# Performance work log

Hardware: AMD Instinct MI355X
Metric: run time of the kernel (lower is better)

## Reference

```python
import jax, jax.numpy as jnp
import numpy as np

LOD = 64          # latent observation dim
LSD = 2 * LOD     # latent state dim
BW = 3            # bandwidth
NB = 15           # num basis
B = 4096          # batch
H = 64            # hidden units of coefficient net

# band-structure indices (static, computed once)
_mask = np.triu(np.ones((LOD, LOD), np.float32), -BW) * np.tril(np.ones((LOD, LOD), np.float32), BW)
IDX0, IDX1 = np.where(_mask == 1)
DIAG_IDX = np.where(IDX0 == IDX1)[0]
NE = IDX0.shape[0]  # = 436 for lod=64, bw=3


def setup_inputs() -> dict:
    key = jax.random.key(0)
    ks = jax.random.split(key, 20)
    inp = {
        'prior_mean': jax.random.normal(ks[0], (B, LSD), jnp.float32),
        'cov_u': jax.random.uniform(ks[1], (B, LOD), jnp.float32) + 0.1,
        'cov_l': jax.random.uniform(ks[2], (B, LOD), jnp.float32) + 0.1,
        'cov_s': 0.1 * jax.random.uniform(ks[3], (B, LOD), jnp.float32),
        'obs': jax.random.normal(ks[4], (B, LOD), jnp.float32),
        'obs_var': jax.random.uniform(ks[5], (B, LOD), jnp.float32) + 0.1,
        # coefficient net params (Linear(LSD,H)-Tanh-Linear(H,H)-Tanh-Linear(H,NB)-Softmax)
        'W1': 0.05 * jax.random.normal(ks[6], (H, LSD), jnp.float32),
        'b1': jnp.zeros((H,), jnp.float32),
        'W2': 0.05 * jax.random.normal(ks[7], (H, H), jnp.float32),
        'b2': jnp.zeros((H,), jnp.float32),
        'W3': 0.05 * jax.random.normal(ks[8], (NB, H), jnp.float32),
        'b3': jnp.zeros((NB,), jnp.float32),
    }
    # transition basis matrices, flat band entries [NB, NE]
    tm11 = 0.02 * jax.random.normal(ks[9], (NB, NE), jnp.float32)
    tm12 = 0.02 * jax.random.normal(ks[10], (NB, NE), jnp.float32)
    tm12 = tm12.at[:, DIAG_IDX].add(0.2)
    tm21 = 0.02 * jax.random.normal(ks[11], (NB, NE), jnp.float32)
    tm21 = tm21.at[:, DIAG_IDX].add(-0.2)
    tm22 = 0.02 * jax.random.normal(ks[12], (NB, NE), jnp.float32)
    inp['tm11_basis'] = tm11
    inp['tm12_basis'] = tm12
    inp['tm21_basis'] = tm21
    inp['tm22_basis'] = tm22
    # log transition noise, init at var_activation_inverse(0.1) = log(exp(0.1)-1)
    inp['log_trans_noise'] = jnp.full((1, LSD), np.log(np.exp(0.1) - 1.0), jnp.float32)
    return inp


def _bmv(mat, vec):
    return jnp.einsum('bij,bj->bi', mat, vec)


def _unflatten_tm(flat):
    # flat: [B, NE] -> banded [B, LOD, LOD]
    tm = jnp.zeros((flat.shape[0], LOD, LOD), flat.dtype)
    return tm.at[:, IDX0, IDX1].set(flat)


def reference(prior_mean, cov_u, cov_l, cov_s, obs, obs_var,
              W1, b1, W2, b2, W3, b3,
              tm11_basis, tm12_basis, tm21_basis, tm22_basis, log_trans_noise):
    # ---- update (Kalman-style, factorized diagonal covariance) ----
    denom = cov_u + obs_var
    q_upper = cov_u / denom
    q_lower = cov_s / denom
    residual = obs - prior_mean[:, :LOD]
    post_mean = prior_mean + jnp.concatenate([q_upper * residual, q_lower * residual], -1)
    covar_factor = 1.0 - q_upper
    post_cu = covar_factor * cov_u
    post_cl = cov_l - q_lower * cov_s
    post_cs = covar_factor * cov_s

    # ---- coefficient net: MLP + softmax -> basis mixing coefficients ----
    h = jnp.tanh(post_mean @ W1.T + b1)
    h = jnp.tanh(h @ W2.T + b2)
    coeff = jax.nn.softmax(h @ W3.T + b3, axis=-1)  # [B, NB]

    # ---- locally-linear transition model ----
    tm11_flat = jnp.einsum('bk,ke->be', coeff, tm11_basis).at[:, DIAG_IDX].add(1.0)
    tm12_flat = jnp.einsum('bk,ke->be', coeff, tm12_basis)
    tm21_flat = jnp.einsum('bk,ke->be', coeff, tm21_basis)
    tm22_flat = jnp.einsum('bk,ke->be', coeff, tm22_basis).at[:, DIAG_IDX].add(1.0)
    tm11 = _unflatten_tm(tm11_flat)
    tm12 = _unflatten_tm(tm12_flat)
    tm21 = _unflatten_tm(tm21_flat)
    tm22 = _unflatten_tm(tm22_flat)

    trans_cov = jnp.log(jnp.exp(log_trans_noise) + 1.0)  # var_activation (softplus)
    tcu = trans_cov[:, :LOD]
    tcl = trans_cov[:, LOD:]

    # ---- predict ----
    mu = post_mean[:, :LOD]
    ml = post_mean[:, LOD:]
    next_mean = jnp.concatenate([_bmv(tm11, mu) + _bmv(tm12, ml),
                                 _bmv(tm21, mu) + _bmv(tm22, ml)], -1)
    # dadat(A, d) = bmv(A^2, d); dadbt(A, d, B) = bmv(A*B, d)
    next_cu = (_bmv(jnp.square(tm11), post_cu) + 2.0 * _bmv(tm11 * tm12, post_cs)
               + _bmv(jnp.square(tm12), post_cl) + tcu)
    next_cl = (_bmv(jnp.square(tm21), post_cu) + 2.0 * _bmv(tm21 * tm22, post_cs)
               + _bmv(jnp.square(tm22), post_cl) + tcl)
    next_cs = (_bmv(tm21 * tm11, post_cu) + _bmv(tm22 * tm11, post_cs)
               + _bmv(tm21 * tm12, post_cs) + _bmv(tm22 * tm12, post_cl))

    return (post_mean, post_cu, post_cl, post_cs, next_mean, next_cu, next_cl, next_cs)
```

## Files before the change

kernel.cpp:

```cpp
#include <hip/hip_runtime.h>
#include <math.h>

#define O_PM   0
#define O_PCU  524288
#define O_PCL  786432
#define O_PCS  1048576
#define O_NM   1310720
#define O_NCU  1835008
#define O_NCL  2097152
#define O_NCS  2359296

#define TM_S   1748
#define L_W1   0
#define L_W2   4864
#define L_W3   7680
#define L_TM   0
#define L_BAST 13984
#define L_PMB  27968
#define L_H1   29184
#define L_H2   29888
#define L_COEF 30592
#define L_PMF  30752
#define L_CUF  32800
#define L_CLF  33824
#define L_CSF  34848
#define L_TOT  35872

typedef short s8v __attribute__((ext_vector_type(8)));
typedef short s4v __attribute__((ext_vector_type(4)));
typedef float f4v __attribute__((ext_vector_type(4)));

__device__ __forceinline__ unsigned pk2(float a, float b) {
    unsigned ua = __float_as_uint(a), ub = __float_as_uint(b);
    ua += 0x7fffu + ((ua >> 16) & 1u);
    ub += 0x7fffu + ((ub >> 16) & 1u);
    return (ua >> 16) | (ub & 0xffff0000u);
}
__device__ __forceinline__ unsigned short tobf(float a) {
    unsigned ua = __float_as_uint(a);
    ua += 0x7fffu + ((ua >> 16) & 1u);
    return (unsigned short)(ua >> 16);
}
__device__ __forceinline__ float frombf(unsigned short u) {
    return __uint_as_float(((unsigned)u) << 16);
}
__device__ __forceinline__ float lo16(unsigned w) { return __uint_as_float(w << 16); }
__device__ __forceinline__ float hi16(unsigned w) { return __uint_as_float(w & 0xffff0000u); }
__device__ __forceinline__ float frcp(float x) { return __builtin_amdgcn_rcpf(x); }
__device__ __forceinline__ float ftanh(float x) {
    float e = __expf(2.f * x);
    return 1.f - 2.f * frcp(e + 1.f);
}
#define SWZ(v, imm) __uint_as_float((unsigned)__builtin_amdgcn_ds_swizzle((int)__float_as_uint(v), imm))

#if __has_builtin(__builtin_amdgcn_mfma_f32_16x16x16_bf16)
#define MFMA16(A,B,C) __builtin_amdgcn_mfma_f32_16x16x16_bf16(A,B,C,0,0,0)
#define HAVE_MFMA16 1
#elif __has_builtin(__builtin_amdgcn_mfma_f32_16x16x16bf16_1k)
#define MFMA16(A,B,C) __builtin_amdgcn_mfma_f32_16x16x16bf16_1k(A,B,C,0,0,0)
#define HAVE_MFMA16 1
#else
#define MFMA16(A,B,C) (C)
#define HAVE_MFMA16 1
#endif

__global__ __launch_bounds__(1024, 4)
void rkn_kernel(const float* __restrict__ prior_mean,
                const float* __restrict__ cov_u,
                const float* __restrict__ cov_l,
                const float* __restrict__ cov_s,
                const float* __restrict__ obs,
                const float* __restrict__ obs_var,
                const float* __restrict__ W1,
                const float* __restrict__ b1,
                const float* __restrict__ W2,
                const float* __restrict__ b2,
                const float* __restrict__ W3,
                const float* __restrict__ b3,
                const float* __restrict__ tm11b,
                const float* __restrict__ tm12b,
                const float* __restrict__ tm21b,
                const float* __restrict__ tm22b,
                const float* __restrict__ ltn,
                float* __restrict__ out)
{
    __shared__ __align__(16) unsigned smem[L_TOT];

    const int tid  = threadIdx.x;
    const int wid  = tid >> 6;
    const int lane = tid & 63;
    const int lrow = lane & 15;
    const int lkg  = lane >> 4;

    {
#pragma unroll
        for (int it = 0; it < 2; ++it) {
            const int idx = it * 1024 + tid;
            const float4 v = ((const float4*)W1)[idx];
            const int j = idx >> 5, kq = idx & 31;
            unsigned* d = smem + (L_W1 + j * 76 + kq * 2);
            d[0] = pk2(v.x, v.y); d[1] = pk2(v.z, v.w);
        }
        {
            const int idx = tid;
            const float4 v = ((const float4*)W2)[idx];
            const int j = idx >> 4, kq = idx & 15;
            unsigned* d = smem + (L_W2 + j * 44 + kq * 2);
            d[0] = pk2(v.x, v.y); d[1] = pk2(v.z, v.w);
        }
        if (tid < 240) {
            const float4 v = ((const float4*)W3)[tid];
            const int j = tid >> 4, kq = tid & 15;
            unsigned* d = smem + (L_W3 + j * 44 + kq * 2);
            d[0] = pk2(v.x, v.y); d[1] = pk2(v.z, v.w);
        } else if (tid < 284) {
            smem[L_W3 + 15 * 44 + (tid - 240)] = 0u;
        }
    }

    if (tid < 512) {
        const int prow  = tid >> 5;
        const int pd    = (tid & 31) << 1;
        const int grow1 = blockIdx.x * 16 + prow;
        const float2 cu2 = *(const float2*)(cov_u   + grow1 * 64 + pd);
        const float2 cl2 = *(const float2*)(cov_l   + grow1 * 64 + pd);
        const float2 cs2 = *(const float2*)(cov_s   + grow1 * 64 + pd);
        const float2 ob2 = *(const float2*)(obs     + grow1 * 64 + pd);
        const float2 ov2 = *(const float2*)(obs_var + grow1 * 64 + pd);
        const float2 pu2 = *(const float2*)(prior_mean + grow1 * 128 + pd);
        const float2 pl2 = *(const float2*)(prior_mean + grow1 * 128 + 64 + pd);

        const float i0 = frcp(cu2.x + ov2.x), i1 = frcp(cu2.y + ov2.y);
        const float qu0 = cu2.x * i0, qu1 = cu2.y * i1;
        const float ql0 = cs2.x * i0, ql1 = cs2.y * i1;
        const float r0 = ob2.x - pu2.x, r1 = ob2.y - pu2.y;
        const float pmu0 = pu2.x + qu0 * r0, pmu1 = pu2.y + qu1 * r1;
        const float pml0 = pl2.x + ql0 * r0, pml1 = pl2.y + ql1 * r1;
        const float cf0 = 1.f - qu0, cf1 = 1.f - qu1;
        const float pcu0 = cf0 * cu2.x, pcu1 = cf1 * cu2.y;
        const float pcl0 = cl2.x - ql0 * cs2.x, pcl1 = cl2.y - ql1 * cs2.y;
        const float pcs0 = cf0 * cs2.x, pcs1 = cf1 * cs2.y;

        *(float2*)(out + O_PM  + grow1 * 128 + pd)      = make_float2(pmu0, pmu1);
        *(float2*)(out + O_PM  + grow1 * 128 + 64 + pd) = make_float2(pml0, pml1);
        *(float2*)(out + O_PCU + grow1 * 64 + pd) = make_float2(pcu0, pcu1);
        *(float2*)(out + O_PCL + grow1 * 64 + pd) = make_float2(pcl0, pcl1);
        *(float2*)(out + O_PCS + grow1 * 64 + pd) = make_float2(pcs0, pcs1);

        smem[L_PMB + prow * 76 + (pd >> 1)]      = pk2(pmu0, pmu1);
        smem[L_PMB + prow * 76 + 32 + (pd >> 1)] = pk2(pml0, pml1);
        *(float2*)((float*)(smem + L_PMF) + prow * 128 + pd)      = make_float2(pmu0, pmu1);
        *(float2*)((float*)(smem + L_PMF) + prow * 128 + 64 + pd) = make_float2(pml0, pml1);
        *(float2*)((float*)(smem + L_CUF) + prow * 64 + pd) = make_float2(pcu0, pcu1);
        *(float2*)((float*)(smem + L_CLF) + prow * 64 + pd) = make_float2(pcl0, pcl1);
        *(float2*)((float*)(smem + L_CSF) + prow * 64 + pd) = make_float2(pcs0, pcs1);
    }

    const float tcu = __logf(__expf(ltn[lane]) + 1.f);
    const float tcl = __logf(__expf(ltn[64 + lane]) + 1.f);

    __syncthreads();

    const int t2 = tid - 256;
    const int ms = t2 & 3;
    const float* bps = (ms == 0) ? tm11b : (ms == 1) ? tm12b : (ms == 2) ? tm21b : tm22b;

    if (wid < 4) {
        const int w = wid;
        f4v acc = {0.f, 0.f, 0.f, 0.f};
#pragma unroll
        for (int s = 0; s < 4; ++s) {
            s8v a = *(const s8v*)(smem + L_PMB + lrow * 76 + s * 16 + lkg * 4);
            s8v b = *(const s8v*)(smem + L_W1 + (w * 16 + lrow) * 76 + s * 16 + lkg * 4);
            acc = __builtin_amdgcn_mfma_f32_16x16x32_bf16(a, b, acc, 0, 0, 0);
        }
        const float bc1 = b1[w * 16 + lrow];
        unsigned short* h1u = (unsigned short*)(smem + L_H1);
#pragma unroll
        for (int q = 0; q < 4; ++q)
            h1u[(lkg * 4 + q) * 88 + w * 16 + lrow] = tobf(ftanh(acc[q] + bc1));
    } else {
#pragma unroll
        for (int kp = 0; kp < 3; ++kp)
#pragma unroll
            for (int c = 0; c < 3; ++c) {
                const int n = c * 768 + t2;
                if (n < 1744) {
                    const int e = n >> 2;
                    const float lo = bps[(2 * kp) * 436 + e];
                    const float hi = bps[(2 * kp + 1) * 436 + e];
                    smem[L_BAST + kp * TM_S + n] = pk2(lo, hi);
                }
            }
    }
    __syncthreads();

    if (wid < 4) {
        const int w = wid;
        f4v acc = {0.f, 0.f, 0.f, 0.f};
#pragma unroll
        for (int s = 0; s < 2; ++s) {
            s8v a = *(const s8v*)(smem + L_H1 + lrow * 44 + s * 16 + lkg * 4);
            s8v b = *(const s8v*)(smem + L_W2 + (w * 16 + lrow) * 44 + s * 16 + lkg * 4);
            acc = __builtin_amdgcn_mfma_f32_16x16x32_bf16(a, b, acc, 0, 0, 0);
        }
        const float bc2 = b2[w * 16 + lrow];
        unsigned short* h2u = (unsigned short*)(smem + L_H2);
#pragma unroll
        for (int q = 0; q < 4; ++q)
            h2u[(lkg * 4 + q) * 88 + w * 16 + lrow] = tobf(ftanh(acc[q] + bc2));
    } else {
#pragma unroll
        for (int kp = 3; kp < 6; ++kp)
#pragma unroll
            for (int c = 0; c < 3; ++c) {
                const int n = c * 768 + t2;
                if (n < 1744) {
                    const int e = n >> 2;
                    const float lo = bps[(2 * kp) * 436 + e];
                    const float hi = bps[(2 * kp + 1) * 436 + e];
                    smem[L_BAST + kp * TM_S + n] = pk2(lo, hi);
                }
            }
    }
    __syncthreads();

    if (wid == 0) {
        f4v acc = {0.f, 0.f, 0.f, 0.f};
#pragma unroll
        for (int s = 0; s < 2; ++s) {
            s8v a = *(const s8v*)(smem + L_H2 + lrow * 44 + s * 16 + lkg * 4);
            s8v b = *(const s8v*)(smem + L_W3 + lrow * 44 + s * 16 + lkg * 4);
            acc = __builtin_amdgcn_mfma_f32_16x16x32_bf16(a, b, acc, 0, 0, 0);
        }
        const float bc3 = (lrow < 15) ? b3[lrow] : 0.f;
        unsigned short* cfu = (unsigned short*)(smem + L_COEF);
#pragma unroll
        for (int q = 0; q < 4; ++q) {
            const float lg = acc[q] + bc3;
            float v = (lrow < 15) ? lg : -1e30f;
            v = fmaxf(v, SWZ(v, 0x041F));
            v = fmaxf(v, SWZ(v, 0x081F));
            v = fmaxf(v, SWZ(v, 0x101F));
            v = fmaxf(v, SWZ(v, 0x201F));
            const float ex = (lrow < 15) ? __expf(lg - v) : 0.f;
            float ss = ex;
            ss += SWZ(ss, 0x041F);
            ss += SWZ(ss, 0x081F);
            ss += SWZ(ss, 0x101F);
            ss += SWZ(ss, 0x201F);
            cfu[(lkg * 4 + q) * 20 + lrow] = tobf(ex * frcp(ss));
        }
    } else if (wid >= 4) {
#pragma unroll
        for (int kp = 6; kp < 8; ++kp)
#pragma unroll
            for (int c = 0; c < 3; ++c) {
                const int n = c * 768 + t2;
                if (n < 1744) {
                    const int e = n >> 2;
                    const float lo = bps[(2 * kp) * 436 + e];
                    const float hi = (kp < 7) ? bps[(2 * kp + 1) * 436 + e] : 0.f;
                    smem[L_BAST + kp * TM_S + n] = pk2(lo, hi);
                }
            }
    }
    __syncthreads();

    {
        unsigned short* tmu = (unsigned short*)(smem + L_TM);
        const s4v ca = *(const s4v*)(smem + L_COEF + lrow * 10 + lkg * 2);
#pragma unroll
        for (int i = 0; i < 7; ++i) {
            const int t = i * 16 + wid;
            if (t < 109) {
                const int nn = t * 16 + lrow;
                unsigned wpair[2];
                wpair[0] = smem[L_BAST + (lkg * 2    ) * TM_S + nn];
                wpair[1] = smem[L_BAST + (lkg * 2 + 1) * TM_S + nn];
                const s4v bb = *(const s4v*)wpair;
                f4v d = {0.f, 0.f, 0.f, 0.f};
                d = MFMA16(ca, bb, d);
#pragma unroll
                for (int q = 0; q < 4; ++q)
                    tmu[(lkg * 4 + q) * TM_S + nn] = tobf(d[q]);
            }
        }
    }
    __syncthreads();

    {
        const int i   = lane;
        const int jlo = (i - 3 > 0) ? (i - 3) : 0;
        const int ne  = ((i + 3 < 63) ? (i + 3) : 63) - jlo + 1;
        const int base = (i < 4)  ? (i * (i + 7)) / 2
                       : (i <= 61) ? (7 * i - 6)
                       : (i == 62) ? 427 : 432;
        const float* pmf = (const float*)(smem + L_PMF);
        const float* cuf = (const float*)(smem + L_CUF);
        const float* clf = (const float*)(smem + L_CLF);
        const float* csf = (const float*)(smem + L_CSF);
        const uint2* tmr = (const uint2*)smem;

        const int r  = wid;
        const int gr = blockIdx.x * 16 + r;
        float nmu = 0.f, nml = 0.f, ncu = 0.f, ncl = 0.f, ncs = 0.f;
#pragma unroll
        for (int dd = 0; dd < 7; ++dd) {
            if (dd < ne) {
                const int j = jlo + dd;
                const uint2 tv = tmr[r * (TM_S / 4) + base + dd];
                float t11 = lo16(tv.x);
                float t12 = hi16(tv.x);
                float t21 = lo16(tv.y);
                float t22 = hi16(tv.y);
                if (j == i) { t11 += 1.f; t22 += 1.f; }
                const float mu  = pmf[r * 128 + j];
                const float ml  = pmf[r * 128 + 64 + j];
                const float vcu = cuf[r * 64 + j];
                const float vcl = clf[r * 64 + j];
                const float vcs = csf[r * 64 + j];
                nmu += t11 * mu + t12 * ml;
                nml += t21 * mu + t22 * ml;
                ncu += t11 * t11 * vcu + 2.f * t11 * t12 * vcs + t12 * t12 * vcl;
                ncl += t21 * t21 * vcu + 2.f * t21 * t22 * vcs + t22 * t22 * vcl;
                ncs += t21 * t11 * vcu + (t22 * t11 + t21 * t12) * vcs + t22 * t12 * vcl;
            }
        }
        out[O_NM  + gr * 128 + i]      = nmu;
        out[O_NM  + gr * 128 + 64 + i] = nml;
        out[O_NCU + gr * 64 + i] = ncu + tcu;
        out[O_NCL + gr * 64 + i] = ncl + tcl;
        out[O_NCS + gr * 64 + i] = ncs;
    }
}

extern "C" void kernel_launch(void* const* d_in, const int* in_sizes, int n_in,
                              void* d_out, int out_size, void* d_ws, size_t ws_size,
                              hipStream_t stream) {
    rkn_kernel<<<dim3(256), dim3(1024), 0, stream>>>(
        (const float*)d_in[0],
        (const float*)d_in[1],
        (const float*)d_in[2],
        (const float*)d_in[3],
        (const float*)d_in[4],
        (const float*)d_in[5],
        (const float*)d_in[6],
        (const float*)d_in[7],
        (const float*)d_in[8],
        (const float*)d_in[9],
        (const float*)d_in[10],
        (const float*)d_in[11],
        (const float*)d_in[12],
        (const float*)d_in[13],
        (const float*)d_in[14],
        (const float*)d_in[15],
        (const float*)d_in[16],
        (float*)d_out);
}
```

Before: 16.93 us.

## Halve block size, split basis contraction in two passes, shrink LDS with bf16 staging

```diff
diff --git a/kernel.cpp b/kernel.cpp
--- a/kernel.cpp
+++ b/kernel.cpp
@@ -15,16 +15,14 @@
 #define L_W2   4864
 #define L_W3   7680
 #define L_TM   0
-#define L_BAST 13984
-#define L_PMB  27968
-#define L_H1   29184
-#define L_H2   29888
-#define L_COEF 30592
-#define L_PMF  30752
-#define L_CUF  32800
-#define L_CLF  33824
-#define L_CSF  34848
-#define L_TOT  35872
+#define L_BAST 8384
+#define L_PMB  15376
+#define L_H1   16592
+#define L_H2   17296
+#define L_COEF 18000
+#define L_CUV  18160
+#define L_CSV  18672
+#define L_TOT  18928
 
 typedef short s8v __attribute__((ext_vector_type(8)));
 typedef short s4v __attribute__((ext_vector_type(4)));
@@ -55,16 +53,13 @@
 
 #if __has_builtin(__builtin_amdgcn_mfma_f32_16x16x16_bf16)
 #define MFMA16(A,B,C) __builtin_amdgcn_mfma_f32_16x16x16_bf16(A,B,C,0,0,0)
-#define HAVE_MFMA16 1
 #elif __has_builtin(__builtin_amdgcn_mfma_f32_16x16x16bf16_1k)
 #define MFMA16(A,B,C) __builtin_amdgcn_mfma_f32_16x16x16bf16_1k(A,B,C,0,0,0)
-#define HAVE_MFMA16 1
 #else
 #define MFMA16(A,B,C) (C)
-#define HAVE_MFMA16 1
 #endif
 
-__global__ __launch_bounds__(1024, 4)
+__global__ __launch_bounds__(512, 4)
 void rkn_kernel(const float* __restrict__ prior_mean,
                 const float* __restrict__ cov_u,
                 const float* __restrict__ cov_l,
@@ -91,18 +86,20 @@
     const int lane = tid & 63;
     const int lrow = lane & 15;
     const int lkg  = lane >> 4;
-
-    {
-#pragma unroll
-        for (int it = 0; it < 2; ++it) {
-            const int idx = it * 1024 + tid;
+    const int row  = blockIdx.x * 8 + wid;
+
+    {
+#pragma unroll
+        for (int it = 0; it < 4; ++it) {
+            const int idx = it * 512 + tid;
             const float4 v = ((const float4*)W1)[idx];
             const int j = idx >> 5, kq = idx & 31;
             unsigned* d = smem + (L_W1 + j * 76 + kq * 2);
             d[0] = pk2(v.x, v.y); d[1] = pk2(v.z, v.w);
         }
-        {
-            const int idx = tid;
+#pragma unroll
+        for (int it = 0; it < 2; ++it) {
+            const int idx = it * 512 + tid;
             const float4 v = ((const float4*)W2)[idx];
             const int j = idx >> 4, kq = idx & 15;
             unsigned* d = smem + (L_W2 + j * 44 + kq * 2);
@@ -118,42 +115,47 @@
         }
     }
 
-    if (tid < 512) {
-        const int prow  = tid >> 5;
-        const int pd    = (tid & 31) << 1;
-        const int grow1 = blockIdx.x * 16 + prow;
-        const float2 cu2 = *(const float2*)(cov_u   + grow1 * 64 + pd);
-        const float2 cl2 = *(const float2*)(cov_l   + grow1 * 64 + pd);
-        const float2 cs2 = *(const float2*)(cov_s   + grow1 * 64 + pd);
-        const float2 ob2 = *(const float2*)(obs     + grow1 * 64 + pd);
-        const float2 ov2 = *(const float2*)(obs_var + grow1 * 64 + pd);
-        const float2 pu2 = *(const float2*)(prior_mean + grow1 * 128 + pd);
-        const float2 pl2 = *(const float2*)(prior_mean + grow1 * 128 + 64 + pd);
-
-        const float i0 = frcp(cu2.x + ov2.x), i1 = frcp(cu2.y + ov2.y);
-        const float qu0 = cu2.x * i0, qu1 = cu2.y * i1;
-        const float ql0 = cs2.x * i0, ql1 = cs2.y * i1;
-        const float r0 = ob2.x - pu2.x, r1 = ob2.y - pu2.y;
-        const float pmu0 = pu2.x + qu0 * r0, pmu1 = pu2.y + qu1 * r1;
-        const float pml0 = pl2.x + ql0 * r0, pml1 = pl2.y + ql1 * r1;
-        const float cf0 = 1.f - qu0, cf1 = 1.f - qu1;
-        const float pcu0 = cf0 * cu2.x, pcu1 = cf1 * cu2.y;
-        const float pcl0 = cl2.x - ql0 * cs2.x, pcl1 = cl2.y - ql1 * cs2.y;
-        const float pcs0 = cf0 * cs2.x, pcs1 = cf1 * cs2.y;
-
-        *(float2*)(out + O_PM  + grow1 * 128 + pd)      = make_float2(pmu0, pmu1);
-        *(float2*)(out + O_PM  + grow1 * 128 + 64 + pd) = make_float2(pml0, pml1);
-        *(float2*)(out + O_PCU + grow1 * 64 + pd) = make_float2(pcu0, pcu1);
-        *(float2*)(out + O_PCL + grow1 * 64 + pd) = make_float2(pcl0, pcl1);
-        *(float2*)(out + O_PCS + grow1 * 64 + pd) = make_float2(pcs0, pcs1);
-
-        smem[L_PMB + prow * 76 + (pd >> 1)]      = pk2(pmu0, pmu1);
-        smem[L_PMB + prow * 76 + 32 + (pd >> 1)] = pk2(pml0, pml1);
-        *(float2*)((float*)(smem + L_PMF) + prow * 128 + pd)      = make_float2(pmu0, pmu1);
-        *(float2*)((float*)(smem + L_PMF) + prow * 128 + 64 + pd) = make_float2(pml0, pml1);
-        *(float2*)((float*)(smem + L_CUF) + prow * 64 + pd) = make_float2(pcu0, pcu1);
-        *(float2*)((float*)(smem + L_CLF) + prow * 64 + pd) = make_float2(pcl0, pcl1);
-        *(float2*)((float*)(smem + L_CSF) + prow * 64 + pd) = make_float2(pcs0, pcs1);
+#pragma unroll
+    for (int it = 0; it < 2; ++it) {
+        const int idx = it * 512 + tid;
+        if (idx < 704) {
+            const int w = (idx < 96) ? ((idx / 12) * 76 + 64 + idx % 12)
+                                     : (608 + (idx - 96));
+            smem[L_PMB + w] = 0u;
+        }
+    }
+
+    {
+        const float cu   = cov_u[row * 64 + lane];
+        const float cl   = cov_l[row * 64 + lane];
+        const float cs   = cov_s[row * 64 + lane];
+        const float ob   = obs[row * 64 + lane];
+        const float ov   = obs_var[row * 64 + lane];
+        const float pmu0 = prior_mean[row * 128 + lane];
+        const float pml0 = prior_mean[row * 128 + 64 + lane];
+
+        const float inv = frcp(cu + ov);
+        const float qu  = cu * inv;
+        const float ql  = cs * inv;
+        const float res = ob - pmu0;
+        const float pmu = pmu0 + qu * res;
+        const float pml = pml0 + ql * res;
+        const float cf  = 1.f - qu;
+        const float pcu = cf * cu;
+        const float pcl = cl - ql * cs;
+        const float pcs = cf * cs;
+
+        out[O_PM  + row * 128 + lane]      = pmu;
+        out[O_PM  + row * 128 + 64 + lane] = pml;
+        out[O_PCU + row * 64 + lane] = pcu;
+        out[O_PCL + row * 64 + lane] = pcl;
+        out[O_PCS + row * 64 + lane] = pcs;
+
+        unsigned short* pmb16 = (unsigned short*)(smem + L_PMB);
+        pmb16[wid * 152 + lane]      = tobf(pmu);
+        pmb16[wid * 152 + 64 + lane] = tobf(pml);
+        smem[L_CUV + wid * 64 + lane] = pk2(pcu, pcl);
+        ((unsigned short*)(smem + L_CSV))[wid * 64 + lane] = tobf(pcs);
     }
 
     const float tcu = __logf(__expf(ltn[lane]) + 1.f);
@@ -161,7 +163,7 @@
 
     __syncthreads();
 
-    const int t2 = tid - 256;
+    const int t2 = tid & 255;
     const int ms = t2 & 3;
     const float* bps = (ms == 0) ? tm11b : (ms == 1) ? tm12b : (ms == 2) ? tm21b : tm22b;
 
@@ -181,15 +183,14 @@
             h1u[(lkg * 4 + q) * 88 + w * 16 + lrow] = tobf(ftanh(acc[q] + bc1));
     } else {
 #pragma unroll
-        for (int kp = 0; kp < 3; ++kp)
-#pragma unroll
-            for (int c = 0; c < 3; ++c) {
-                const int n = c * 768 + t2;
+        for (int kp = 0; kp < 2; ++kp)
+#pragma unroll
+            for (int c = 0; c < 7; ++c) {
+                const int n = c * 256 + t2;
                 if (n < 1744) {
                     const int e = n >> 2;
-                    const float lo = bps[(2 * kp) * 436 + e];
-                    const float hi = bps[(2 * kp + 1) * 436 + e];
-                    smem[L_BAST + kp * TM_S + n] = pk2(lo, hi);
+                    smem[L_BAST + kp * TM_S + n] =
+                        pk2(bps[(2 * kp) * 436 + e], bps[(2 * kp + 1) * 436 + e]);
                 }
             }
     }
@@ -211,15 +212,14 @@
             h2u[(lkg * 4 + q) * 88 + w * 16 + lrow] = tobf(ftanh(acc[q] + bc2));
     } else {
 #pragma unroll
-        for (int kp = 3; kp < 6; ++kp)
-#pragma unroll
-            for (int c = 0; c < 3; ++c) {
-                const int n = c * 768 + t2;
+        for (int kp = 2; kp < 4; ++kp)
+#pragma unroll
+            for (int c = 0; c < 7; ++c) {
+                const int n = c * 256 + t2;
                 if (n < 1744) {
                     const int e = n >> 2;
-                    const float lo = bps[(2 * kp) * 436 + e];
-                    const float hi = bps[(2 * kp + 1) * 436 + e];
-                    smem[L_BAST + kp * TM_S + n] = pk2(lo, hi);
+                    smem[L_BAST + kp * TM_S + n] =
+                        pk2(bps[(2 * kp) * 436 + e], bps[(2 * kp + 1) * 436 + e]);
                 }
             }
     }
@@ -251,16 +251,43 @@
             ss += SWZ(ss, 0x201F);
             cfu[(lkg * 4 + q) * 20 + lrow] = tobf(ex * frcp(ss));
         }
-    } else if (wid >= 4) {
-#pragma unroll
-        for (int kp = 6; kp < 8; ++kp)
-#pragma unroll
-            for (int c = 0; c < 3; ++c) {
-                const int n = c * 768 + t2;
+    }
+    __syncthreads();
+
+    f4v d[14];
+#pragma unroll
+    for (int i = 0; i < 14; ++i) d[i] = (f4v){0.f, 0.f, 0.f, 0.f};
+    {
+        s4v ca = (s4v){0, 0, 0, 0};
+        if (lkg < 2) ca = *(const s4v*)(smem + L_COEF + lrow * 10 + lkg * 2);
+#pragma unroll
+        for (int i = 0; i < 14; ++i) {
+            const int t = i * 8 + wid;
+            if (t < 109) {
+                const int nn = t * 16 + lrow;
+                unsigned wp[2] = {0u, 0u};
+                if (lkg < 2) {
+                    wp[0] = smem[L_BAST + (lkg * 2    ) * TM_S + nn];
+                    wp[1] = smem[L_BAST + (lkg * 2 + 1) * TM_S + nn];
+                }
+                d[i] = MFMA16(ca, *(const s4v*)wp, d[i]);
+            }
+        }
+    }
+    __syncthreads();
+
+    {
+        const int mb = tid & 3;
+        const float* bpb = (mb == 0) ? tm11b : (mb == 1) ? tm12b : (mb == 2) ? tm21b : tm22b;
+#pragma unroll
+        for (int kp = 0; kp < 4; ++kp)
+#pragma unroll
+            for (int c = 0; c < 4; ++c) {
+                const int n = c * 512 + tid;
                 if (n < 1744) {
                     const int e = n >> 2;
-                    const float lo = bps[(2 * kp) * 436 + e];
-                    const float hi = (kp < 7) ? bps[(2 * kp + 1) * 436 + e] : 0.f;
+                    const float lo = bpb[(8 + 2 * kp) * 436 + e];
+                    const float hi = (9 + 2 * kp < 15) ? bpb[(9 + 2 * kp) * 436 + e] : 0.f;
                     smem[L_BAST + kp * TM_S + n] = pk2(lo, hi);
                 }
             }
@@ -268,22 +295,25 @@
     __syncthreads();
 
     {
-        unsigned short* tmu = (unsigned short*)(smem + L_TM);
-        const s4v ca = *(const s4v*)(smem + L_COEF + lrow * 10 + lkg * 2);
-#pragma unroll
-        for (int i = 0; i < 7; ++i) {
-            const int t = i * 16 + wid;
+        s4v ca = (s4v){0, 0, 0, 0};
+        if (lkg < 2) ca = *(const s4v*)(smem + L_COEF + lrow * 10 + 4 + lkg * 2);
+        unsigned short* tmu = (unsigned short*)smem;
+#pragma unroll
+        for (int i = 0; i < 14; ++i) {
+            const int t = i * 8 + wid;
             if (t < 109) {
                 const int nn = t * 16 + lrow;
-                unsigned wpair[2];
-                wpair[0] = smem[L_BAST + (lkg * 2    ) * TM_S + nn];
-                wpair[1] = smem[L_BAST + (lkg * 2 + 1) * TM_S + nn];
-                const s4v bb = *(const s4v*)wpair;
-                f4v d = {0.f, 0.f, 0.f, 0.f};
-                d = MFMA16(ca, bb, d);
-#pragma unroll
-                for (int q = 0; q < 4; ++q)
-                    tmu[(lkg * 4 + q) * TM_S + nn] = tobf(d[q]);
+                unsigned wp[2] = {0u, 0u};
+                if (lkg < 2) {
+                    wp[0] = smem[L_BAST + (lkg * 2    ) * TM_S + nn];
+                    wp[1] = smem[L_BAST + (lkg * 2 + 1) * TM_S + nn];
+                }
+                d[i] = MFMA16(ca, *(const s4v*)wp, d[i]);
+                if (lkg < 2) {
+#pragma unroll
+                    for (int q = 0; q < 4; ++q)
+                        tmu[(lkg * 4 + q) * TM_S + nn] = tobf(d[i][q]);
+                }
             }
         }
     }
@@ -296,14 +326,11 @@
         const int base = (i < 4)  ? (i * (i + 7)) / 2
                        : (i <= 61) ? (7 * i - 6)
                        : (i == 62) ? 427 : 432;
-        const float* pmf = (const float*)(smem + L_PMF);
-        const float* cuf = (const float*)(smem + L_CUF);
-        const float* clf = (const float*)(smem + L_CLF);
-        const float* csf = (const float*)(smem + L_CSF);
+        const unsigned short* pmb16 = (const unsigned short*)(smem + L_PMB);
+        const unsigned short* csv16 = (const unsigned short*)(smem + L_CSV);
         const uint2* tmr = (const uint2*)smem;
 
-        const int r  = wid;
-        const int gr = blockIdx.x * 16 + r;
+        const int r = wid;
         float nmu = 0.f, nml = 0.f, ncu = 0.f, ncl = 0.f, ncs = 0.f;
 #pragma unroll
         for (int dd = 0; dd < 7; ++dd) {
@@ -315,11 +342,12 @@
                 float t21 = lo16(tv.y);
                 float t22 = hi16(tv.y);
                 if (j == i) { t11 += 1.f; t22 += 1.f; }
-                const float mu  = pmf[r * 128 + j];
-                const float ml  = pmf[r * 128 + 64 + j];
-                const float vcu = cuf[r * 64 + j];
-                const float vcl = clf[r * 64 + j];
-                const float vcs = csf[r * 64 + j];
+                const float mu  = frombf(pmb16[r * 152 + j]);
+                const float ml  = frombf(pmb16[r * 152 + 64 + j]);
+                const unsigned cc = smem[L_CUV + r * 64 + j];
+                const float vcu = lo16(cc);
+                const float vcl = hi16(cc);
+                const float vcs = frombf(csv16[r * 64 + j]);
                 nmu += t11 * mu + t12 * ml;
                 nml += t21 * mu + t22 * ml;
                 ncu += t11 * t11 * vcu + 2.f * t11 * t12 * vcs + t12 * t12 * vcl;
@@ -327,18 +355,18 @@
                 ncs += t21 * t11 * vcu + (t22 * t11 + t21 * t12) * vcs + t22 * t12 * vcl;
             }
         }
-        out[O_NM  + gr * 128 + i]      = nmu;
-        out[O_NM  + gr * 128 + 64 + i] = nml;
-        out[O_NCU + gr * 64 + i] = ncu + tcu;
-        out[O_NCL + gr * 64 + i] = ncl + tcl;
-        out[O_NCS + gr * 64 + i] = ncs;
+        out[O_NM  + row * 128 + i]      = nmu;
+        out[O_NM  + row * 128 + 64 + i] = nml;
+        out[O_NCU + row * 64 + i] = ncu + tcu;
+        out[O_NCL + row * 64 + i] = ncl + tcl;
+        out[O_NCS + row * 64 + i] = ncs;
     }
 }
 
 extern "C" void kernel_launch(void* const* d_in, const int* in_sizes, int n_in,
                               void* d_out, int out_size, void* d_ws, size_t ws_size,
                               hipStream_t stream) {
-    rkn_kernel<<<dim3(256), dim3(1024), 0, stream>>>(
+    rkn_kernel<<<dim3(512), dim3(512), 0, stream>>>(
         (const float*)d_in[0],
         (const float*)d_in[1],
         (const float*)d_in[2],
```

After: 21.56 us. +27.3%, slower.
